# Optimization experiments

Measured on AMD Instinct MI355X. Metric: run time of the kernel, lower is better.

The kernel has to match this reference:

```python
import jax, jax.numpy as jnp
import numpy as np

MIN_NORM = 1e-15
BALL_EPS_F32 = 0.004  # BALL_EPS[torch.float32]


def _norm(x):
    return jnp.maximum(jnp.linalg.norm(x, axis=-1, keepdims=True), MIN_NORM)


def project(x, c=1.0):
    norm = _norm(x)
    maxnorm = (1.0 - BALL_EPS_F32) / (c ** 0.5)
    return jnp.where(norm > maxnorm, x / norm * maxnorm, x)


def expmap0(u, c=1.0):
    sqrt_c = c ** 0.5
    un = _norm(u)
    gamma = jnp.tanh(jnp.clip(sqrt_c * un, -15.0, 15.0)) * u / (sqrt_c * un)
    return project(gamma, c)


def artanh(x):
    x = jnp.clip(x, -1.0 + 1e-5, 1.0 - 1e-5)
    return 0.5 * (jnp.log1p(x) - jnp.log1p(-x))


def logmap0(y, c=1.0):
    sqrt_c = c ** 0.5
    yn = _norm(y)
    return y / yn / sqrt_c * artanh(sqrt_c * yn)


def mobius_add(x, y, c=1.0):
    x2 = jnp.sum(x * x, axis=-1, keepdims=True)
    y2 = jnp.sum(y * y, axis=-1, keepdims=True)
    xy = jnp.sum(x * y, axis=-1, keepdims=True)
    num = (1 + 2 * c * xy + c * y2) * x + (1 - c * x2) * y
    denom = 1 + 2 * c * xy + (c ** 2) * x2 * y2
    return num / jnp.maximum(denom, MIN_NORM)


def p_exp_map(v):
    nv = jnp.maximum(jnp.linalg.norm(v, axis=-1, keepdims=True), 1e-10)
    return jnp.tanh(nv) * v / nv


def setup_inputs() -> dict:
    key = jax.random.key(0)
    ks = jax.random.split(key, 16)
    E, N, B = 1_000_000, 100_000, 512
    n_rel, D, A = 200, 64, 5
    R = 2 * n_rel + 1  # 401

    q_sub = jax.random.randint(ks[0], (B,), 0, N, dtype=jnp.int32)
    q_rel = jax.random.randint(ks[1], (B,), 0, R, dtype=jnp.int32)
    hidden = jax.random.normal(ks[2], (N, D), dtype=jnp.float32)

    r_idx = jax.random.randint(ks[3], (E,), 0, B, dtype=jnp.int32)
    rel = jax.random.randint(ks[4], (E,), 0, R, dtype=jnp.int32)
    sub = jax.random.randint(ks[5], (E,), 0, N, dtype=jnp.int32)
    obj = jax.random.randint(ks[6], (E,), 0, N, dtype=jnp.int32)
    dummy = jnp.zeros((E,), dtype=jnp.int32)
    edges = jnp.stack([r_idx, dummy, rel, dummy, sub, obj], axis=1)  # [E,6]

    s = 1.0 / np.sqrt(D)
    sa = 1.0 / np.sqrt(A)
    rela_embed = jax.random.normal(ks[7], (R, D), dtype=jnp.float32)
    query_embed = jax.random.normal(ks[8], (R, D), dtype=jnp.float32)
    Ws = jax.random.uniform(ks[9], (A, D), jnp.float32, -s, s)
    Wr = jax.random.uniform(ks[10], (A, D), jnp.float32, -s, s)
    Wqr_w = jax.random.uniform(ks[11], (A, D), jnp.float32, -s, s)
    Wqr_b = jax.random.uniform(ks[12], (A,), jnp.float32, -s, s)
    walpha_w = jax.random.uniform(ks[13], (1, A), jnp.float32, -sa, sa)
    walpha_b = jax.random.uniform(ks[14], (1,), jnp.float32, -sa, sa)
    Wh = jax.random.uniform(ks[15], (D, D), jnp.float32, -s, s)

    return {
        "q_sub": q_sub, "q_rel": q_rel, "hidden": hidden, "edges": edges,
        "n_node": N, "old_nodes_new_idx": jax.random.randint(jax.random.fold_in(key, 99), (100,), 0, N, dtype=jnp.int32),
        "rela_embed": rela_embed, "query_embed": query_embed,
        "Ws": Ws, "Wr": Wr, "Wqr_w": Wqr_w, "Wqr_b": Wqr_b,
        "walpha_w": walpha_w, "walpha_b": walpha_b, "Wh": Wh,
    }


def reference(q_sub, q_rel, hidden, edges, n_node, old_nodes_new_idx,
              rela_embed, query_embed, Ws, Wr, Wqr_w, Wqr_b,
              walpha_w, walpha_b, Wh):
    sub = edges[:, 4]
    rel = edges[:, 2]
    obj = edges[:, 5]
    r_idx = edges[:, 0]

    hs = hidden[sub]                     # [E, D] gather
    hr = rela_embed[rel]                 # [E, D]
    h_qr = query_embed[q_rel][r_idx]     # [E, D]

    # attention (note: bilinear/non_linear branch in the original is dead code)
    pre = hs @ Ws.T + hr @ Wr.T + (h_qr @ Wqr_w.T + Wqr_b)   # [E, A]
    alpha = jax.nn.sigmoid(jax.nn.relu(pre) @ walpha_w.T + walpha_b)  # [E, 1]

    hr_h = expmap0(hr, 1.0)
    hs_h = expmap0(hs, 1.0)
    message = logmap0(project(mobius_add(hs_h, hr_h, 1.0), 1.0), 1.0)
    message = alpha * message            # [E, D]

    message_agg = jax.ops.segment_sum(message, obj, num_segments=n_node)  # [N, D]
    a = message_agg @ Wh.T
    a = p_exp_map(a)
    hidden_new = logmap0(a, 1.0)         # act is identity
    return hidden_new
```

## Files before the change

kernel.cpp:

```cpp
#include <hip/hip_runtime.h>
#include <hip/hip_bf16.h>
#include <hip/hip_fp16.h>


__device__ __forceinline__ float wave_sum(float v) {
#pragma unroll
    for (int off = 32; off > 0; off >>= 1) v += __shfl_xor(v, off, 64);
    return v;
}

__device__ __forceinline__ float frcp(float x) {
#if __has_builtin(__builtin_amdgcn_rcpf)
    return __builtin_amdgcn_rcpf(x);
#else
    return 1.f / x;
#endif
}
__device__ __forceinline__ float fsqrt_(float x) {
#if __has_builtin(__builtin_amdgcn_sqrtf)
    return __builtin_amdgcn_sqrtf(x);
#else
    return sqrtf(x);
#endif
}
__device__ __forceinline__ float flog2_(float x) {
#if __has_builtin(__builtin_amdgcn_logf)
    return __builtin_amdgcn_logf(x);
#else
    return log2f(x);
#endif
}
__device__ __forceinline__ float fexp2_(float x) {
#if __has_builtin(__builtin_amdgcn_exp2f)
    return __builtin_amdgcn_exp2f(x);
#else
    return exp2f(x);
#endif
}
__device__ __forceinline__ float ftanh_pos(float x) {
    return 1.f - 2.f * frcp(fexp2_(x * 2.885390082f) + 1.f);
}

__device__ __forceinline__ unsigned pk2(float a, float b) {
    __half2 h = __floats2half2_rn(a, b);
    return __builtin_bit_cast(unsigned, h);
}
__device__ __forceinline__ float2 upk2(unsigned u) {
    __half2 h = __builtin_bit_cast(__half2, u);
    return __half22float2(h);
}

__device__ __forceinline__ void expmap0_scale(float norm, float& s, float& x2) {
    const float maxn = 1.0f - 0.004f;
    float un = fmaxf(norm, 1e-15f);
    float th = ftanh_pos(fminf(un, 15.0f));
    float gs = th * frcp(un);
    float ng = gs * norm;
    float ps = ng > maxn ? maxn * frcp(ng) : 1.0f;
    s = gs * ps;
    float sn = s * norm;
    x2 = sn * sn;
}

__device__ __forceinline__ float2 edge_coef(
    unsigned hu_lo, unsigned hu_hi, unsigned yu_lo, unsigned yu_hi,
    uint4 hsa, uint4 hra, uint4 pqa, const float* wa, float wb) {
    float2 hs01 = upk2(hsa.x), hs23 = upk2(hsa.y), hs4 = upk2(hsa.z), hsxs = upk2(hsa.w);
    float2 hr01 = upk2(hra.x), hr23 = upk2(hra.y), hr4 = upk2(hra.z), hry = upk2(hra.w);
    float2 pq01 = upk2(pqa.x), pq23 = upk2(pqa.y), pq4 = upk2(pqa.z);
    float x2 = hsxs.x, s = hsxs.y, y2 = hry.x;

    float2 hl = upk2(hu_lo), hh = upk2(hu_hi);
    float2 yl = upk2(yu_lo), yh = upk2(yu_hi);

    float p = hl.x * yl.x;
    p = fmaf(hl.y, yl.y, p);
    p = fmaf(hh.x, yh.x, p);
    p = fmaf(hh.y, yh.y, p);
    p += __shfl_xor(p, 1, 64);
    p += __shfl_xor(p, 2, 64);
    p += __shfl_xor(p, 4, 64);
    p += __shfl_xor(p, 8, 64);
    float xy = p * s;

    float z = wb;
    z = fmaf(fmaxf(hs01.x + hr01.x + pq01.x, 0.f), wa[0], z);
    z = fmaf(fmaxf(hs01.y + hr01.y + pq01.y, 0.f), wa[1], z);
    z = fmaf(fmaxf(hs23.x + hr23.x + pq23.x, 0.f), wa[2], z);
    z = fmaf(fmaxf(hs23.y + hr23.y + pq23.y, 0.f), wa[3], z);
    z = fmaf(fmaxf(hs4.x + hr4.x + pq4.x, 0.f), wa[4], z);
    float alpha = frcp(1.f + fexp2_(z * -1.44269504f));

    float Af  = 1.f + 2.f * xy + y2;
    float Bf  = 1.f - x2;
    float den = fmaxf(1.f + 2.f * xy + x2 * y2, 1e-15f);
    float inv = frcp(den);
    float nm2 = fmaxf(fmaf(Af * Af, x2, fmaf(2.f * Af * Bf, xy, Bf * Bf * y2)), 0.f);
    float nm  = fsqrt_(nm2) * inv;
    const float maxn = 1.0f - 0.004f;
    float ps  = nm > maxn ? maxn * frcp(nm) : 1.f;
    float yn  = fmaxf(fminf(nm, maxn), 1e-15f);
    float ratio = (1.f + yn) * frcp(1.f - yn);
    float art = 0.34657359f * flog2_(ratio);
    float k  = inv * ps * alpha * art * frcp(yn);
    return make_float2(k * Af * s, k * Bf);
}

__device__ __forceinline__ void edge_to_global(
    unsigned hu_lo, unsigned hu_hi, unsigned yu_lo, unsigned yu_hi,
    uint4 hsa, uint4 hra, uint4 pqa, const float* wa, float wb,
    bool act, __half2* dst ) {
    float2 c = edge_coef(hu_lo, hu_hi, yu_lo, yu_hi, hsa, hra, pqa, wa, wb);
    float2 hl = upk2(hu_lo), hh = upk2(hu_hi);
    float2 yl = upk2(yu_lo), yh = upk2(yu_hi);
    __half2 q_lo = __floats2half2_rn(fmaf(c.x, hl.x, c.y * yl.x), fmaf(c.x, hl.y, c.y * yl.y));
    __half2 q_hi = __floats2half2_rn(fmaf(c.x, hh.x, c.y * yh.x), fmaf(c.x, hh.y, c.y * yh.y));
    if (act) {
        unsafeAtomicAdd(dst, q_lo);
        unsafeAtomicAdd(dst + 16, q_hi);
    }
}

__global__ void prep_fused16(const int* __restrict__ q_rel,
                             const float* __restrict__ query_embed,
                             const float* __restrict__ Wqr_w,
                             const float* __restrict__ Wqr_b,
                             const float* __restrict__ rela_embed,
                             const float* __restrict__ Wr,
                             const float* __restrict__ hidden,
                             const float* __restrict__ Ws,
                             const int* __restrict__ edges,
                             __half* __restrict__ hidden16,
                             uint4* __restrict__ hs_aux16,
                             __half* __restrict__ hr_h16,
                             uint4* __restrict__ hr_aux16,
                             uint4* __restrict__ preq16,
                             __half* __restrict__ agg16,
                             unsigned long long* __restrict__ packed,
                             int N, int R, int B, int E, int zero_agg) {
    int wid = (blockIdx.x * blockDim.x + threadIdx.x) >> 6;
    int lane = threadIdx.x & 63;
    int nwaves = (N + 3) >> 2;
    if (wid < nwaves) {
        int q = lane >> 4, j = lane & 15;
        int n = wid * 4 + q;
        bool act = n < N;
        int nc = act ? n : N - 1;

        float4 u = *(const float4*)(hidden + (size_t)nc * 64 + 4 * j);
        float4 w0 = *(const float4*)(Ws + 0 * 64 + 4 * j);
        float4 w1 = *(const float4*)(Ws + 1 * 64 + 4 * j);
        float4 w2 = *(const float4*)(Ws + 2 * 64 + 4 * j);
        float4 w3 = *(const float4*)(Ws + 3 * 64 + 4 * j);
        float4 w4 = *(const float4*)(Ws + 4 * 64 + 4 * j);

#define DOT4(a, b) (fmaf((a).x, (b).x, fmaf((a).y, (b).y, fmaf((a).z, (b).z, (a).w * (b).w))))
        float p0 = DOT4(u, u);
        float p1 = DOT4(u, w0);
        float p2 = DOT4(u, w1);
        float p3 = DOT4(u, w2);
        float p4 = DOT4(u, w3);
        float p5 = DOT4(u, w4);
#undef DOT4
#pragma unroll
        for (int off = 1; off < 16; off <<= 1) {
            p0 += __shfl_xor(p0, off, 64);
            p1 += __shfl_xor(p1, off, 64);
            p2 += __shfl_xor(p2, off, 64);
            p3 += __shfl_xor(p3, off, 64);
            p4 += __shfl_xor(p4, off, 64);
            p5 += __shfl_xor(p5, off, 64);
        }
        float s, x2;
        expmap0_scale(fsqrt_(p0), s, x2);
        if (act) {
            uint2 hp; hp.x = pk2(u.x, u.y); hp.y = pk2(u.z, u.w);
            *(uint2*)(hidden16 + (size_t)n * 64 + 4 * j) = hp;
            if (zero_agg) {
                uint2 zz; zz.x = 0u; zz.y = 0u;
                ((uint2*)(agg16 + (size_t)n * 64))[j] = zz;
            }
            if (j == 0) {
                uint4 o; o.x = pk2(p1, p2); o.y = pk2(p3, p4); o.z = pk2(p5, 0.f); o.w = pk2(x2, s);
                hs_aux16[n] = o;
            }
        }
        return;
    }
    int w2 = wid - nwaves;
    if (w2 < R) {
        int r = w2;
        float u = rela_embed[r * 64 + lane];
        float p0 = u * u;
        float p1 = u * Wr[0 * 64 + lane];
        float p2 = u * Wr[1 * 64 + lane];
        float p3 = u * Wr[2 * 64 + lane];
        float p4 = u * Wr[3 * 64 + lane];
        float p5 = u * Wr[4 * 64 + lane];
#pragma unroll
        for (int off = 1; off < 64; off <<= 1) {
            p0 += __shfl_xor(p0, off, 64);
            p1 += __shfl_xor(p1, off, 64);
            p2 += __shfl_xor(p2, off, 64);
            p3 += __shfl_xor(p3, off, 64);
            p4 += __shfl_xor(p4, off, 64);
            p5 += __shfl_xor(p5, off, 64);
        }
        float s, y2;
        expmap0_scale(fsqrt_(p0), s, y2);
        hr_h16[r * 64 + lane] = __float2half(s * u);
        if (lane == 0) {
            uint4 o; o.x = pk2(p1, p2); o.y = pk2(p3, p4); o.z = pk2(p5, 0.f); o.w = pk2(y2, 0.f);
            hr_aux16[r] = o;
        }
        return;
    }
    int w3 = w2 - R;
    if (w3 < B) {
        int b = w3;
        int qr = q_rel[b];
        float q = query_embed[qr * 64 + lane];
        float p1 = q * Wqr_w[0 * 64 + lane];
        float p2 = q * Wqr_w[1 * 64 + lane];
        float p3 = q * Wqr_w[2 * 64 + lane];
        float p4 = q * Wqr_w[3 * 64 + lane];
        float p5 = q * Wqr_w[4 * 64 + lane];
#pragma unroll
        for (int off = 1; off < 64; off <<= 1) {
            p1 += __shfl_xor(p1, off, 64);
            p2 += __shfl_xor(p2, off, 64);
            p3 += __shfl_xor(p3, off, 64);
            p4 += __shfl_xor(p4, off, 64);
            p5 += __shfl_xor(p5, off, 64);
        }
        if (lane == 0) {
            uint4 o;
            o.x = pk2(p1 + Wqr_b[0], p2 + Wqr_b[1]);
            o.y = pk2(p3 + Wqr_b[2], p4 + Wqr_b[3]);
            o.z = pk2(p5 + Wqr_b[4], 0.f);
            o.w = pk2(0.f, 0.f);
            preq16[b] = o;
        }
        return;
    }
    int w4 = w3 - B;
    int e = w4 * 64 + lane;
    if (e < E) {
        const int* er = edges + (size_t)e * 6;
        int ri  = er[0];
        int rel = er[2];
        int sub = er[4];
        int obj = er[5];
        unsigned long long pk = (unsigned long long)(unsigned)(obj & 0x1ffff)
            | ((unsigned long long)(unsigned)(sub & 0x1ffff) << 17)
            | ((unsigned long long)(unsigned)(rel & 0x1ff) << 34)
            | ((unsigned long long)(unsigned)(ri & 0x1ff) << 43);
        __builtin_nontemporal_store(pk, &packed[e]);
    }
}


__global__ void init_cur(int* __restrict__ cur, int NB, int cap) {
    int i = blockIdx.x * blockDim.x + threadIdx.x;
    if (i < NB) cur[i] = i * cap;
    else if (i == NB) cur[i] = 0;
}

__global__ __launch_bounds__(256) void scatter_edges(
    const int* __restrict__ edges, int E, int NB, int cap,
    int* __restrict__ cur,
    unsigned long long* __restrict__ bbuf,
    unsigned long long* __restrict__ ovfbuf, int ovfcap)
{
    __shared__ unsigned long long spk[4096];
    __shared__ int lh[1024];
    __shared__ int lb[1024];
    int t = threadIdx.x;
    int base = blockIdx.x * 4096;
    for (int i = t; i < NB; i += 256) lh[i] = 0;
    __syncthreads();
    int nloc = min(4096, E - base);
    for (int k = t; k < nloc; k += 256) {
        const long long* er = (const long long*)(edges + (size_t)(base + k) * 6);
        long long a = er[0], bq = er[1], cq = er[2];
        int ri = (int)a, rel = (int)bq, sub = (int)cq, obj = (int)(cq >> 32);
        unsigned long long pk = (unsigned long long)(unsigned)(obj & 0x1ffff)
            | ((unsigned long long)(unsigned)(sub & 0x1ffff) << 17)
            | ((unsigned long long)(unsigned)(rel & 0x1ff) << 34)
            | ((unsigned long long)(unsigned)(ri & 0x1ff) << 43);
        spk[k] = pk;
        atomicAdd(&lh[obj >> 7], 1);
    }
    __syncthreads();
    for (int i = t; i < NB; i += 256) {
        int c = lh[i];
        lb[i] = c ? atomicAdd(&cur[i], c) : 0;
    }
    __syncthreads();
    for (int i = t; i < NB; i += 256) lh[i] = 0;
    __syncthreads();
    for (int k = t; k < nloc; k += 256) {
        unsigned long long pk = spk[k];
        int bk = (int)(pk & 0x1ffff) >> 7;
        int rank = atomicAdd(&lh[bk], 1);
        int slot = lb[bk] + rank;
        if (slot < (bk + 1) * cap) {
            bbuf[slot] = pk;
        } else {
            int o = atomicAdd(cur + NB, 1);
            if (o < ovfcap) ovfbuf[o] = pk;
        }
    }
}

__global__ __launch_bounds__(256) void sort_bucket(
    unsigned long long* __restrict__ bbuf,
    const int* __restrict__ cur, int cap,
    int2* __restrict__ nodeoff)
{
    __shared__ unsigned long long spk[4096];
    __shared__ int hist[128];
    __shared__ int pfx[129];
    __shared__ int rk[128];
    int b = blockIdx.x;
    int t = threadIdx.x;
    int start = b * cap;
    int cnt = cur[b] - start;
    if (cnt < 0) cnt = 0;
    if (cnt > cap) cnt = cap;
    if (t < 128) { hist[t] = 0; rk[t] = 0; }
    __syncthreads();
    for (int i = t; i < cnt; i += 256) {
        unsigned long long pk = bbuf[start + i];
        spk[i] = pk;
        atomicAdd(&hist[(int)(pk & 127)], 1);
    }
    __syncthreads();
    if (t == 0) {
        int acc = 0;
#pragma unroll 4
        for (int i = 0; i < 128; ++i) { pfx[i] = acc; acc += hist[i]; }
        pfx[128] = acc;
    }
    __syncthreads();
    if (t < 128) {
        nodeoff[b * 128 + t] = make_int2(start + pfx[t], start + pfx[t + 1]);
    }
    for (int i = t; i < cnt; i += 256) {
        unsigned long long pk = spk[i];
        int loc = (int)(pk & 127);
        int r = atomicAdd(&rk[loc], 1);
        bbuf[start + pfx[loc] + r] = pk;
    }
}

__global__ __launch_bounds__(256) void csr_edge(
    const unsigned long long* __restrict__ bbuf,
    const int2* __restrict__ nodeoff,
    const __half* __restrict__ hidden16,
    const __half* __restrict__ hr_h16,
    const uint4* __restrict__ hs_aux16,
    const uint4* __restrict__ hr_aux16,
    const uint4* __restrict__ preq16,
    const float* __restrict__ walpha_w,
    const float* __restrict__ walpha_b,
    __half* __restrict__ agg16,
    int N, int Ntot)
{
    int t = threadIdx.x;
    int lane = t & 63;
    int g = lane >> 4;
    int j = lane & 15;
    int node = blockIdx.x * 16 + (t >> 6) * 4 + g;
    if (node >= Ntot) return;

    float wa[5];
    wa[0] = walpha_w[0]; wa[1] = walpha_w[1]; wa[2] = walpha_w[2];
    wa[3] = walpha_w[3]; wa[4] = walpha_w[4];
    float wb = walpha_b[0];

    int2 off = nodeoff[node];
    float a0 = 0.f, a1 = 0.f, a2 = 0.f, a3 = 0.f;
    for (int e = off.x; e < off.y; ++e) {
        unsigned long long pk = bbuf[e];
        int sub = (int)((pk >> 17) & 0x1ffff);
        int rel = (int)((pk >> 34) & 0x1ff);
        int ri  = (int)((pk >> 43) & 0x1ff);
        uint4 hsa = hs_aux16[sub], hra = hr_aux16[rel], pqa = preq16[ri];
        const unsigned* hrow = (const unsigned*)(hidden16 + (size_t)sub * 64);
        const unsigned* yrow = (const unsigned*)(hr_h16 + (size_t)rel * 64);
        unsigned hu_lo = hrow[j], hu_hi = hrow[16 + j];
        unsigned yu_lo = yrow[j], yu_hi = yrow[16 + j];
        float2 c = edge_coef(hu_lo, hu_hi, yu_lo, yu_hi, hsa, hra, pqa, wa, wb);
        float2 hl = upk2(hu_lo), hh = upk2(hu_hi);
        float2 yl = upk2(yu_lo), yh = upk2(yu_hi);
        a0 = fmaf(c.x, hl.x, fmaf(c.y, yl.x, a0));
        a1 = fmaf(c.x, hl.y, fmaf(c.y, yl.y, a1));
        a2 = fmaf(c.x, hh.x, fmaf(c.y, yh.x, a2));
        a3 = fmaf(c.x, hh.y, fmaf(c.y, yh.y, a3));
    }
    if (node < N) {
        unsigned* dst = (unsigned*)(agg16 + (size_t)node * 64);
        __builtin_nontemporal_store(pk2(a0, a1), dst + j);
        __builtin_nontemporal_store(pk2(a2, a3), dst + 16 + j);
    }
}

__global__ __launch_bounds__(256) void ovf_edge(
    const unsigned long long* __restrict__ ovfbuf,
    const int* __restrict__ ovfcnt_p, int ovfcap,
    const __half* __restrict__ hidden16,
    const __half* __restrict__ hr_h16,
    const uint4* __restrict__ hs_aux16,
    const uint4* __restrict__ hr_aux16,
    const uint4* __restrict__ preq16,
    const float* __restrict__ walpha_w,
    const float* __restrict__ walpha_b,
    __half2* __restrict__ agg)
{
    int cnt = min(*ovfcnt_p, ovfcap);
    if (cnt <= 0) return;
    int j = threadIdx.x & 15;
    int qid = (blockIdx.x * blockDim.x + threadIdx.x) >> 4;
    int nq = (gridDim.x * blockDim.x) >> 4;
    float wa[5];
    wa[0] = walpha_w[0]; wa[1] = walpha_w[1]; wa[2] = walpha_w[2];
    wa[3] = walpha_w[3]; wa[4] = walpha_w[4];
    float wb = walpha_b[0];
    for (int e = qid; e < cnt; e += nq) {
        unsigned long long pk = ovfbuf[e];
        int obj = (int)(pk & 0x1ffff), sub = (int)((pk >> 17) & 0x1ffff);
        int rel = (int)((pk >> 34) & 0x1ff), ri = (int)((pk >> 43) & 0x1ff);
        uint4 hsa = hs_aux16[sub], hra = hr_aux16[rel], pqa = preq16[ri];
        const unsigned* hrow = (const unsigned*)(hidden16 + (size_t)sub * 64);
        const unsigned* yrow = (const unsigned*)(hr_h16 + (size_t)rel * 64);
        edge_to_global(hrow[j], hrow[16 + j], yrow[j], yrow[16 + j],
                       hsa, hra, pqa, wa, wb, true, agg + (size_t)obj * 32 + j);
    }
}

__global__ __launch_bounds__(256) void edge_kernel8p(
    const unsigned long long* __restrict__ packed,
    const __half* __restrict__ hidden16,
    const __half* __restrict__ hr_h16,
    const uint4* __restrict__ hs_aux16,
    const uint4* __restrict__ hr_aux16,
    const uint4* __restrict__ preq16,
    const float* __restrict__ walpha_w,
    const float* __restrict__ walpha_b,
    __half2* __restrict__ agg,
    int E)
{
    int wid = (blockIdx.x * blockDim.x + threadIdx.x) >> 6;
    int lane = threadIdx.x & 63;
    int g = lane >> 4;
    int j = lane & 15;

    int e0 = wid * 8 + g;
    int e1 = wid * 8 + 4 + g;
    bool act0 = e0 < E, act1 = e1 < E;

    unsigned long long p0 = __builtin_nontemporal_load(&packed[act0 ? e0 : 0]);
    unsigned long long p1 = __builtin_nontemporal_load(&packed[act1 ? e1 : 0]);
    int obj0 = (int)(p0 & 0x1ffff), sub0 = (int)((p0 >> 17) & 0x1ffff);
    int rel0 = (int)((p0 >> 34) & 0x1ff), r0 = (int)((p0 >> 43) & 0x1ff);
    int obj1 = (int)(p1 & 0x1ffff), sub1 = (int)((p1 >> 17) & 0x1ffff);
    int rel1 = (int)((p1 >> 34) & 0x1ff), r1 = (int)((p1 >> 43) & 0x1ff);

    uint4 hsa0 = hs_aux16[sub0], hra0 = hr_aux16[rel0], pqa0 = preq16[r0];
    uint4 hsa1 = hs_aux16[sub1], hra1 = hr_aux16[rel1], pqa1 = preq16[r1];

    const unsigned* hrow0 = (const unsigned*)(hidden16 + (size_t)sub0 * 64);
    const unsigned* yrow0 = (const unsigned*)(hr_h16 + (size_t)rel0 * 64);
    const unsigned* hrow1 = (const unsigned*)(hidden16 + (size_t)sub1 * 64);
    const unsigned* yrow1 = (const unsigned*)(hr_h16 + (size_t)rel1 * 64);

    float wa[5];
    wa[0] = walpha_w[0]; wa[1] = walpha_w[1]; wa[2] = walpha_w[2];
    wa[3] = walpha_w[3]; wa[4] = walpha_w[4];
    float wb = walpha_b[0];

    edge_to_global(hrow0[j], hrow0[16 + j], yrow0[j], yrow0[16 + j],
                   hsa0, hra0, pqa0, wa, wb, act0, agg + (size_t)obj0 * 32 + j);
    edge_to_global(hrow1[j], hrow1[16 + j], yrow1[j], yrow1[16 + j],
                   hsa1, hra1, pqa1, wa, wb, act1, agg + (size_t)obj1 * 32 + j);
}

__global__ __launch_bounds__(256) void final_gemm16(
    float* __restrict__ out,
    const __half* __restrict__ agg16,
    const float* __restrict__ Wh,
    int N)
{
    __shared__ __half tile[64 * 64];
    int t = threadIdx.x;
    int lane = t & 63;
    int w = t >> 6;

    float wh[64];
    const float4* whr = (const float4*)(Wh + (size_t)lane * 64);
#pragma unroll
    for (int i = 0; i < 16; ++i) {
        float4 v = whr[i];
        wh[4 * i] = v.x; wh[4 * i + 1] = v.y; wh[4 * i + 2] = v.z; wh[4 * i + 3] = v.w;
    }

    int base = blockIdx.x << 6;
    int nrow = min(64, N - base);
    {
        const uint2* src = (const uint2*)(agg16 + (size_t)base * 64);
        uint2* dst = (uint2*)tile;
        int nu2 = nrow * 16;
        for (int i = t; i < nu2; i += 256) dst[i] = src[i];
    }
    __syncthreads();

#pragma unroll 1
    for (int r = 0; r < 16; ++r) {
        int n = base + w * 16 + r;
        if (n >= N) break;
        const uint2* arow = (const uint2*)(tile + (w * 16 + r) * 64);
        float acc = 0.f;
#pragma unroll
        for (int kk = 0; kk < 16; ++kk) {
            uint2 u = arow[kk];
            float2 f0 = upk2(u.x), f1 = upk2(u.y);
            acc = fmaf(f0.x, wh[4 * kk], acc);
            acc = fmaf(f0.y, wh[4 * kk + 1], acc);
            acc = fmaf(f1.x, wh[4 * kk + 2], acc);
            acc = fmaf(f1.y, wh[4 * kk + 3], acc);
        }
        float n2 = wave_sum(acc * acc);
        float na = fsqrt_(n2);
        float nv = fmaxf(na, 1e-10f);
        float pn = ftanh_pos(nv);
        float rinv = frcp(nv);
        float pp = pn * acc * rinv;
        float np = pn * (na * rinv);
        float yn = fmaxf(np, 1e-15f);
        float tt = fminf(yn, 1.f - 1e-5f);
        float ratio = (1.f + tt) * frcp(1.f - tt);
        float art = 0.34657359f * flog2_(ratio);
        __builtin_nontemporal_store(pp * art * frcp(yn), &out[(size_t)n * 64 + lane]);
    }
}


__global__ void prep_small_kernel(const int* __restrict__ q_rel,
                                  const float* __restrict__ query_embed,
                                  const float* __restrict__ Wqr_w,
                                  const float* __restrict__ Wqr_b,
                                  const float* __restrict__ rela_embed,
                                  const float* __restrict__ Wr,
                                  float* __restrict__ hr_h,
                                  float* __restrict__ hr_aux,
                                  float* __restrict__ preq,
                                  int R, int B, int A) {
    int w = (blockIdx.x * blockDim.x + threadIdx.x) >> 6;
    int lane = threadIdx.x & 63;
    if (w < R) {
        int r = w;
        float u = rela_embed[r * 64 + lane];
        float n2 = wave_sum(u * u);
        float s, y2;
        expmap0_scale(fsqrt_(n2), s, y2);
        hr_h[r * 64 + lane] = s * u;
        for (int a = 0; a < A; ++a) {
            float p = wave_sum(u * Wr[a * 64 + lane]);
            if (lane == 0) hr_aux[r * 8 + a] = p;
        }
        if (lane == 0) hr_aux[r * 8 + 6] = y2;
    } else if (w < R + B) {
        int b = w - R;
        int qr = q_rel[b];
        float q = query_embed[qr * 64 + lane];
        for (int a = 0; a < A; ++a) {
            float p = wave_sum(q * Wqr_w[a * 64 + lane]);
            if (lane == 0) preq[b * 8 + a] = p + Wqr_b[a];
        }
    }
}

__global__ void prep_node_kernel(const float* __restrict__ hidden,
                                 const float* __restrict__ Ws,
                                 float* __restrict__ hs_aux, int N, int A) {
    int w = (blockIdx.x * blockDim.x + threadIdx.x) >> 6;
    if (w >= N) return;
    int lane = threadIdx.x & 63;
    float u = hidden[(size_t)w * 64 + lane];
    float n2 = wave_sum(u * u);
    float s, x2;
    expmap0_scale(fsqrt_(n2), s, x2);
    for (int a = 0; a < A; ++a) {
        float p = wave_sum(u * Ws[a * 64 + lane]);
        if (lane == 0) hs_aux[w * 8 + a] = p;
    }
    if (lane == 0) { hs_aux[w * 8 + 6] = x2; hs_aux[w * 8 + 7] = s; }
}

__global__ void edge_kernel_f32(const int* __restrict__ edges,
                                const float* __restrict__ hidden,
                                const float* __restrict__ hr_h,
                                const float* __restrict__ hr_aux,
                                const float* __restrict__ hs_aux,
                                const float* __restrict__ preq,
                                const float* __restrict__ walpha_w,
                                const float* __restrict__ walpha_b,
                                float* __restrict__ agg,
                                int E, int A) {
    int w = (blockIdx.x * blockDim.x + threadIdx.x) >> 6;
    if (w >= E) return;
    int lane = threadIdx.x & 63;
    const int* er = edges + (size_t)w * 6;
    int r_idx = er[0], rel = er[2], sub = er[4], obj = er[5];

    float s  = hs_aux[(size_t)sub * 8 + 7];
    float x2 = hs_aux[(size_t)sub * 8 + 6];
    float h  = hidden[(size_t)sub * 64 + lane];
    float x  = h * s;
    float y  = hr_h[(size_t)rel * 64 + lane];
    float y2 = hr_aux[(size_t)rel * 8 + 6];
    float xy = wave_sum(x * y);

    float z = walpha_b[0];
    for (int a = 0; a < A; ++a) {
        float pre = hs_aux[(size_t)sub * 8 + a] + hr_aux[(size_t)rel * 8 + a] + preq[(size_t)r_idx * 8 + a];
        z += fmaxf(pre, 0.f) * walpha_w[a];
    }
    float alpha = frcp(1.f + fexp2_(z * -1.44269504f));

    float Af = 1.f + 2.f * xy + y2;
    float Bf = 1.f - x2;
    float den = fmaxf(1.f + 2.f * xy + x2 * y2, 1e-15f);
    float inv = frcp(den);
    float nm2 = fmaxf(Af * Af * x2 + 2.f * Af * Bf * xy + Bf * Bf * y2, 0.f);
    float nm = fsqrt_(nm2) * inv;
    const float maxn = 1.0f - 0.004f;
    float ps = nm > maxn ? maxn * frcp(nm) : 1.f;
    float yn = fmaxf(fminf(nm, maxn), 1e-15f);
    float ratio = (1.f + yn) * frcp(1.f - yn);
    float art = 0.34657359f * flog2_(ratio);
    float k = inv * ps * alpha * art * frcp(yn);
    float msg = fmaf(k * Af * s, h, k * Bf * y);
    unsafeAtomicAdd(agg + (size_t)obj * 64 + lane, msg);
}

__global__ void final_kernel_f32(float* __restrict__ out,
                                 const float* __restrict__ Wh,
                                 int N) {
    __shared__ float WhT[64 * 64];
    int t = threadIdx.x;
    for (int i = t; i < 64 * 64; i += blockDim.x) {
        int row = i >> 6, col = i & 63;
        WhT[col * 64 + row] = Wh[i];
    }
    __syncthreads();

    int lane = t & 63;
    int wl = t >> 6;
    int wpb = blockDim.x >> 6;
    int wg = blockIdx.x * wpb + wl;
    int wstride = gridDim.x * wpb;

    for (int n = wg; n < N; n += wstride) {
        float v = out[(size_t)n * 64 + lane];
        float a = 0.f;
#pragma unroll
        for (int k = 0; k < 64; ++k)
            a = fmaf(__shfl(v, k, 64), WhT[k * 64 + lane], a);

        float n2 = wave_sum(a * a);
        float na = fsqrt_(n2);
        float nv = fmaxf(na, 1e-10f);
        float pn = tanhf(nv);
        float rinv = frcp(nv);
        float pp = pn * a * rinv;
        float np = pn * (na * rinv);
        float yn = fmaxf(np, 1e-15f);
        float tt = fminf(yn, 1.f - 1e-5f);
        float ratio = (1.f + tt) * frcp(1.f - tt);
        float art = 0.34657359f * flog2_(ratio);
        out[(size_t)n * 64 + lane] = pp * art * frcp(yn);
    }
}

extern "C" void kernel_launch(void* const* d_in, const int* in_sizes, int n_in,
                              void* d_out, int out_size, void* d_ws, size_t ws_size,
                              hipStream_t stream) {
    const int*   q_rel       = (const int*)d_in[1];
    const float* hidden      = (const float*)d_in[2];
    const int*   edges       = (const int*)d_in[3];
    const float* rela_embed  = (const float*)d_in[6];
    const float* query_embed = (const float*)d_in[7];
    const float* Ws          = (const float*)d_in[8];
    const float* Wr          = (const float*)d_in[9];
    const float* Wqr_w       = (const float*)d_in[10];
    const float* Wqr_b       = (const float*)d_in[11];
    const float* walpha_w    = (const float*)d_in[12];
    const float* walpha_b    = (const float*)d_in[13];
    const float* Wh          = (const float*)d_in[14];

    const int D = 64;
    int B = in_sizes[0];
    int E = in_sizes[3] / 6;
    int A = in_sizes[11];
    int R = in_sizes[6] / D;
    int N = out_size / D;

    float* out = (float*)d_out;

    size_t agg_b    = (size_t)N * 128;
    size_t hid16_b  = (size_t)N * 128;
    size_t hsaux_b  = (size_t)N * 16;
    size_t hrh_b    = (size_t)R * 128;
    size_t hraux_b  = (size_t)R * 16;
    size_t preq_b   = (size_t)B * 16;
    size_t need16   = agg_b + hid16_b + hsaux_b + hrh_b + hraux_b + preq_b;
    size_t packed_b = (size_t)E * 8;
    size_t need_pk  = need16 + packed_b;

    int NB = (N + 127) >> 7;
    int Ntot = NB * 128;
    int cap = (NB > 0) ? 2 * ((E + NB - 1) / NB) : 512;
    if (cap < 512) cap = 512;
    int ovfcap = 65536;
    size_t bbuf_b = (size_t)NB * (size_t)cap * 8;
    size_t cur_b  = (((size_t)NB + 1) * 4 + 15) & ~(size_t)15;
    size_t noff_b = (size_t)Ntot * 8;
    size_t ovf_b  = (size_t)ovfcap * 8;
    size_t need_csr = need16 + bbuf_b + cur_b + noff_b + ovf_b;

    bool fields_ok = (N > 0) && (N <= 131072) && (R <= 512) && (B <= 512);
    bool csr_ok = (A == 5) && fields_ok && (NB <= 1024) && (E > 0) &&
                  (cap <= 4096) && ((long long)NB * cap < (1LL << 31)) &&
                  (ws_size >= need_csr);
    bool pkpath = (A == 5) && fields_ok && (ws_size >= need_pk);

    if (csr_ok) {
        char* base = (char*)d_ws;
        __half* agg16    = (__half*)base;            base += agg_b;
        __half* hidden16 = (__half*)base;            base += hid16_b;
        uint4*  hs_aux16 = (uint4*)base;             base += hsaux_b;
        __half* hr_h16   = (__half*)base;            base += hrh_b;
        uint4*  hr_aux16 = (uint4*)base;             base += hraux_b;
        uint4*  preq16   = (uint4*)base;             base += preq_b;
        unsigned long long* bbuf = (unsigned long long*)base; base += bbuf_b;
        int* cur = (int*)base;                       base += cur_b;
        int2* nodeoff = (int2*)base;                 base += noff_b;
        unsigned long long* ovfbuf = (unsigned long long*)base;

        init_cur<<<(NB + 1 + 255) / 256, 256, 0, stream>>>(cur, NB, cap);

        int nwaves = (N + 3) / 4;
        int total_waves = nwaves + R + B;
        prep_fused16<<<(total_waves + 3) / 4, 256, 0, stream>>>(
            q_rel, query_embed, Wqr_w, Wqr_b, rela_embed, Wr,
            hidden, Ws, edges, hidden16, hs_aux16, hr_h16, hr_aux16, preq16,
            agg16, (unsigned long long*)nullptr, N, R, B, 0, 0);

        scatter_edges<<<(E + 4095) / 4096, 256, 0, stream>>>(
            edges, E, NB, cap, cur, bbuf, ovfbuf, ovfcap);

        sort_bucket<<<NB, 256, 0, stream>>>(bbuf, cur, cap, nodeoff);

        csr_edge<<<(Ntot + 15) / 16, 256, 0, stream>>>(
            bbuf, nodeoff, hidden16, hr_h16, hs_aux16, hr_aux16, preq16,
            walpha_w, walpha_b, agg16, N, Ntot);

        ovf_edge<<<64, 256, 0, stream>>>(
            ovfbuf, cur + NB, ovfcap, hidden16, hr_h16, hs_aux16, hr_aux16,
            preq16, walpha_w, walpha_b, (__half2*)agg16);

        int ntiles = (N + 63) / 64;
        final_gemm16<<<ntiles, 256, 0, stream>>>(out, agg16, Wh, N);
    } else if (pkpath) {
        char* base = (char*)d_ws;
        __half2* agg      = (__half2*)base;          base += agg_b;
        __half*  hidden16 = (__half*)base;           base += hid16_b;
        uint4*   hs_aux16 = (uint4*)base;            base += hsaux_b;
        __half*  hr_h16   = (__half*)base;           base += hrh_b;
        uint4*   hr_aux16 = (uint4*)base;            base += hraux_b;
        uint4*   preq16   = (uint4*)base;            base += preq_b;
        unsigned long long* packed = (unsigned long long*)base;

        int nwaves = (N + 3) / 4;
        int ewavesP = (E + 63) / 64;
        int total_waves = nwaves + R + B + ewavesP;
        prep_fused16<<<(total_waves + 3) / 4, 256, 0, stream>>>(
            q_rel, query_embed, Wqr_w, Wqr_b, rela_embed, Wr,
            hidden, Ws, edges, hidden16, hs_aux16, hr_h16, hr_aux16, preq16,
            (__half*)agg, packed, N, R, B, E, 1);

        int ewaves = (E + 7) / 8;
        edge_kernel8p<<<(ewaves + 3) / 4, 256, 0, stream>>>(
            packed, hidden16, hr_h16, hs_aux16, hr_aux16, preq16,
            walpha_w, walpha_b, agg, E);

        int ntiles = (N + 63) / 64;
        final_gemm16<<<ntiles, 256, 0, stream>>>(out, (const __half*)agg, Wh, N);
    } else {
        float* hs_aux = (float*)d_ws;
        float* hr_h   = hs_aux + (size_t)N * 8;
        float* hr_aux = hr_h + (size_t)R * 64;
        float* preq   = hr_aux + (size_t)R * 8;

        (void)hipMemsetAsync(d_out, 0, (size_t)out_size * sizeof(float), stream);

        int waves_small = R + B;
        prep_small_kernel<<<(waves_small * 64 + 255) / 256, 256, 0, stream>>>(
            q_rel, query_embed, Wqr_w, Wqr_b, rela_embed, Wr,
            hr_h, hr_aux, preq, R, B, A);

        prep_node_kernel<<<(N + 3) / 4, 256, 0, stream>>>(hidden, Ws, hs_aux, N, A);

        edge_kernel_f32<<<(E + 3) / 4, 256, 0, stream>>>(
            edges, hidden, hr_h, hr_aux, hs_aux, preq,
            walpha_w, walpha_b, out, E, A);

        final_kernel_f32<<<1024, 256, 0, stream>>>(out, Wh, N);
    }
}
```

Baseline: 163.2 us.

## Process CSR node edges four-wide per wave with fp32 aux tables and fused cur init

The CSR edge kernel now assigns one node per wave and has its four 16-lane groups process four edges at a time, combining partial sums with cross-group shuffles. Per-node load imbalance and the serial per-edge loop latency should shrink. The per-edge auxiliary projections (hs/hr/query) are now also stored as fp32 float4 pairs, so the edge kernel skips half-precision unpacking at the cost of more gather bytes. The separate init_cur launch is folded into the prep kernel to save one launch, and grid size grows four times.

```diff
diff --git a/kernel.cpp b/kernel.cpp
--- a/kernel.cpp
+++ b/kernel.cpp
@@ -109,7 +109,7 @@
 __device__ __forceinline__ void edge_to_global(
     unsigned hu_lo, unsigned hu_hi, unsigned yu_lo, unsigned yu_hi,
     uint4 hsa, uint4 hra, uint4 pqa, const float* wa, float wb,
-    bool act, __half2* dst ) {
+    bool act, __half2* dst) {
     float2 c = edge_coef(hu_lo, hu_hi, yu_lo, yu_hi, hsa, hra, pqa, wa, wb);
     float2 hl = upk2(hu_lo), hh = upk2(hu_hi);
     float2 yl = upk2(yu_lo), yh = upk2(yu_hi);
@@ -119,6 +119,47 @@
         unsafeAtomicAdd(dst, q_lo);
         unsafeAtomicAdd(dst + 16, q_hi);
     }
+}
+
+__device__ __forceinline__ float2 edge_coef32(
+    unsigned hu_lo, unsigned hu_hi, unsigned yu_lo, unsigned yu_hi,
+    float4 hsA, float4 hsB, float4 hrA, float4 hrB, float4 pqA, float pq5,
+    const float* wa, float wb) {
+    float x2 = hsB.z, s = hsB.w, y2 = hrB.z;
+    float2 hl = upk2(hu_lo), hh = upk2(hu_hi);
+    float2 yl = upk2(yu_lo), yh = upk2(yu_hi);
+
+    float p = hl.x * yl.x;
+    p = fmaf(hl.y, yl.y, p);
+    p = fmaf(hh.x, yh.x, p);
+    p = fmaf(hh.y, yh.y, p);
+    p += __shfl_xor(p, 1, 64);
+    p += __shfl_xor(p, 2, 64);
+    p += __shfl_xor(p, 4, 64);
+    p += __shfl_xor(p, 8, 64);
+    float xy = p * s;
+
+    float z = wb;
+    z = fmaf(fmaxf(hsA.x + hrA.x + pqA.x, 0.f), wa[0], z);
+    z = fmaf(fmaxf(hsA.y + hrA.y + pqA.y, 0.f), wa[1], z);
+    z = fmaf(fmaxf(hsA.z + hrA.z + pqA.z, 0.f), wa[2], z);
+    z = fmaf(fmaxf(hsA.w + hrA.w + pqA.w, 0.f), wa[3], z);
+    z = fmaf(fmaxf(hsB.x + hrB.x + pq5, 0.f), wa[4], z);
+    float alpha = frcp(1.f + fexp2_(z * -1.44269504f));
+
+    float Af  = 1.f + 2.f * xy + y2;
+    float Bf  = 1.f - x2;
+    float den = fmaxf(1.f + 2.f * xy + x2 * y2, 1e-15f);
+    float inv = frcp(den);
+    float nm2 = fmaxf(fmaf(Af * Af, x2, fmaf(2.f * Af * Bf, xy, Bf * Bf * y2)), 0.f);
+    float nm  = fsqrt_(nm2) * inv;
+    const float maxn = 1.0f - 0.004f;
+    float ps  = nm > maxn ? maxn * frcp(nm) : 1.f;
+    float yn  = fmaxf(fminf(nm, maxn), 1e-15f);
+    float ratio = (1.f + yn) * frcp(1.f - yn);
+    float art = 0.34657359f * flog2_(ratio);
+    float k  = inv * ps * alpha * art * frcp(yn);
+    return make_float2(k * Af * s, k * Bf);
 }
 
 __global__ void prep_fused16(const int* __restrict__ q_rel,
@@ -135,9 +176,14 @@
                              __half* __restrict__ hr_h16,
                              uint4* __restrict__ hr_aux16,
                              uint4* __restrict__ preq16,
+                             float4* __restrict__ hs_aux32,
+                             float4* __restrict__ hr_aux32,
+                             float4* __restrict__ preq32,
                              __half* __restrict__ agg16,
                              unsigned long long* __restrict__ packed,
-                             int N, int R, int B, int E, int zero_agg) {
+                             int* __restrict__ cur,
+                             int N, int R, int B, int E, int NB, int cap,
+                             int zero_agg) {
     int wid = (blockIdx.x * blockDim.x + threadIdx.x) >> 6;
     int lane = threadIdx.x & 63;
     int nwaves = (N + 3) >> 2;
@@ -183,6 +229,10 @@
             if (j == 0) {
                 uint4 o; o.x = pk2(p1, p2); o.y = pk2(p3, p4); o.z = pk2(p5, 0.f); o.w = pk2(x2, s);
                 hs_aux16[n] = o;
+                if (hs_aux32) {
+                    hs_aux32[(size_t)n * 2]     = make_float4(p1, p2, p3, p4);
+                    hs_aux32[(size_t)n * 2 + 1] = make_float4(p5, 0.f, x2, s);
+                }
             }
         }
         return;
@@ -212,6 +262,10 @@
         if (lane == 0) {
             uint4 o; o.x = pk2(p1, p2); o.y = pk2(p3, p4); o.z = pk2(p5, 0.f); o.w = pk2(y2, 0.f);
             hr_aux16[r] = o;
+            if (hr_aux32) {
+                hr_aux32[(size_t)r * 2]     = make_float4(p1, p2, p3, p4);
+                hr_aux32[(size_t)r * 2 + 1] = make_float4(p5, 0.f, y2, 0.f);
+            }
         }
         return;
     }
@@ -234,16 +288,25 @@
             p5 += __shfl_xor(p5, off, 64);
         }
         if (lane == 0) {
+            float b1 = p1 + Wqr_b[0], b2 = p2 + Wqr_b[1], b3 = p3 + Wqr_b[2];
+            float b4 = p4 + Wqr_b[3], b5 = p5 + Wqr_b[4];
             uint4 o;
-            o.x = pk2(p1 + Wqr_b[0], p2 + Wqr_b[1]);
-            o.y = pk2(p3 + Wqr_b[2], p4 + Wqr_b[3]);
-            o.z = pk2(p5 + Wqr_b[4], 0.f);
-            o.w = pk2(0.f, 0.f);
+            o.x = pk2(b1, b2); o.y = pk2(b3, b4); o.z = pk2(b5, 0.f); o.w = pk2(0.f, 0.f);
             preq16[b] = o;
+            if (preq32) {
+                preq32[(size_t)b * 2]     = make_float4(b1, b2, b3, b4);
+                preq32[(size_t)b * 2 + 1] = make_float4(b5, 0.f, 0.f, 0.f);
+            }
         }
         return;
     }
     int w4 = w3 - B;
+    if (cur) {
+        int i = w4 * 64 + lane;
+        if (i < NB) cur[i] = i * cap;
+        else if (i == NB) cur[i] = 0;
+        return;
+    }
     int e = w4 * 64 + lane;
     if (e < E) {
         const int* er = edges + (size_t)e * 6;
@@ -259,12 +322,6 @@
     }
 }
 
-
-__global__ void init_cur(int* __restrict__ cur, int NB, int cap) {
-    int i = blockIdx.x * blockDim.x + threadIdx.x;
-    if (i < NB) cur[i] = i * cap;
-    else if (i == NB) cur[i] = 0;
-}
 
 __global__ __launch_bounds__(256) void scatter_edges(
     const int* __restrict__ edges, int E, int NB, int cap,
@@ -354,14 +411,14 @@
     }
 }
 
-__global__ __launch_bounds__(256) void csr_edge(
+__global__ __launch_bounds__(256) void csr_edge_w(
     const unsigned long long* __restrict__ bbuf,
     const int2* __restrict__ nodeoff,
     const __half* __restrict__ hidden16,
     const __half* __restrict__ hr_h16,
-    const uint4* __restrict__ hs_aux16,
-    const uint4* __restrict__ hr_aux16,
-    const uint4* __restrict__ preq16,
+    const float4* __restrict__ hs_aux32,
+    const float4* __restrict__ hr_aux32,
+    const float4* __restrict__ preq32,
     const float* __restrict__ walpha_w,
     const float* __restrict__ walpha_b,
     __half* __restrict__ agg16,
@@ -371,7 +428,7 @@
     int lane = t & 63;
     int g = lane >> 4;
     int j = lane & 15;
-    int node = blockIdx.x * 16 + (t >> 6) * 4 + g;
+    int node = blockIdx.x * 4 + (t >> 6);
     if (node >= Ntot) return;
 
     float wa[5];
@@ -381,25 +438,38 @@
 
     int2 off = nodeoff[node];
     float a0 = 0.f, a1 = 0.f, a2 = 0.f, a3 = 0.f;
-    for (int e = off.x; e < off.y; ++e) {
-        unsigned long long pk = bbuf[e];
+    for (int base = off.x; base < off.y; base += 4) {
+        int e = base + g;
+        bool act = e < off.y;
+        int ec = act ? e : off.y - 1;
+        unsigned long long pk = bbuf[ec];
         int sub = (int)((pk >> 17) & 0x1ffff);
         int rel = (int)((pk >> 34) & 0x1ff);
         int ri  = (int)((pk >> 43) & 0x1ff);
-        uint4 hsa = hs_aux16[sub], hra = hr_aux16[rel], pqa = preq16[ri];
+        float4 hsA = hs_aux32[(size_t)sub * 2], hsB = hs_aux32[(size_t)sub * 2 + 1];
+        float4 hrA = hr_aux32[(size_t)rel * 2], hrB = hr_aux32[(size_t)rel * 2 + 1];
+        float4 pqA = preq32[(size_t)ri * 2],   pqB = preq32[(size_t)ri * 2 + 1];
         const unsigned* hrow = (const unsigned*)(hidden16 + (size_t)sub * 64);
         const unsigned* yrow = (const unsigned*)(hr_h16 + (size_t)rel * 64);
         unsigned hu_lo = hrow[j], hu_hi = hrow[16 + j];
         unsigned yu_lo = yrow[j], yu_hi = yrow[16 + j];
-        float2 c = edge_coef(hu_lo, hu_hi, yu_lo, yu_hi, hsa, hra, pqa, wa, wb);
+        float2 c = edge_coef32(hu_lo, hu_hi, yu_lo, yu_hi,
+                               hsA, hsB, hrA, hrB, pqA, pqB.x, wa, wb);
+        float gate = act ? 1.f : 0.f;
+        float cx = c.x * gate, cy = c.y * gate;
         float2 hl = upk2(hu_lo), hh = upk2(hu_hi);
         float2 yl = upk2(yu_lo), yh = upk2(yu_hi);
-        a0 = fmaf(c.x, hl.x, fmaf(c.y, yl.x, a0));
-        a1 = fmaf(c.x, hl.y, fmaf(c.y, yl.y, a1));
-        a2 = fmaf(c.x, hh.x, fmaf(c.y, yh.x, a2));
-        a3 = fmaf(c.x, hh.y, fmaf(c.y, yh.y, a3));
-    }
-    if (node < N) {
+        a0 = fmaf(cx, hl.x, fmaf(cy, yl.x, a0));
+        a1 = fmaf(cx, hl.y, fmaf(cy, yl.y, a1));
+        a2 = fmaf(cx, hh.x, fmaf(cy, yh.x, a2));
+        a3 = fmaf(cx, hh.y, fmaf(cy, yh.y, a3));
+    }
+    a0 += __shfl_xor(a0, 16, 64); a0 += __shfl_xor(a0, 32, 64);
+    a1 += __shfl_xor(a1, 16, 64); a1 += __shfl_xor(a1, 32, 64);
+    a2 += __shfl_xor(a2, 16, 64); a2 += __shfl_xor(a2, 32, 64);
+    a3 += __shfl_xor(a3, 16, 64); a3 += __shfl_xor(a3, 32, 64);
+
+    if (node < N && g == 0) {
         unsigned* dst = (unsigned*)(agg16 + (size_t)node * 64);
         __builtin_nontemporal_store(pk2(a0, a1), dst + j);
         __builtin_nontemporal_store(pk2(a2, a3), dst + 16 + j);
@@ -709,15 +779,18 @@
 
     float* out = (float*)d_out;
 
-    size_t agg_b    = (size_t)N * 128;
-    size_t hid16_b  = (size_t)N * 128;
-    size_t hsaux_b  = (size_t)N * 16;
-    size_t hrh_b    = (size_t)R * 128;
-    size_t hraux_b  = (size_t)R * 16;
-    size_t preq_b   = (size_t)B * 16;
-    size_t need16   = agg_b + hid16_b + hsaux_b + hrh_b + hraux_b + preq_b;
-    size_t packed_b = (size_t)E * 8;
-    size_t need_pk  = need16 + packed_b;
+    size_t agg_b     = (size_t)N * 128;
+    size_t hid16_b   = (size_t)N * 128;
+    size_t hsaux_b   = (size_t)N * 16;
+    size_t hrh_b     = (size_t)R * 128;
+    size_t hraux_b   = (size_t)R * 16;
+    size_t preq_b    = (size_t)B * 16;
+    size_t hsaux32_b = (size_t)N * 32;
+    size_t hraux32_b = (size_t)R * 32;
+    size_t preq32_b  = (size_t)B * 32;
+    size_t need16    = agg_b + hid16_b + hsaux_b + hrh_b + hraux_b + preq_b;
+    size_t packed_b  = (size_t)E * 8;
+    size_t need_pk   = need16 + packed_b;
 
     int NB = (N + 127) >> 7;
     int Ntot = NB * 128;
@@ -728,7 +801,8 @@
     size_t cur_b  = (((size_t)NB + 1) * 4 + 15) & ~(size_t)15;
     size_t noff_b = (size_t)Ntot * 8;
     size_t ovf_b  = (size_t)ovfcap * 8;
-    size_t need_csr = need16 + bbuf_b + cur_b + noff_b + ovf_b;
+    size_t need_csr = need16 + hsaux32_b + hraux32_b + preq32_b +
+                      bbuf_b + cur_b + noff_b + ovf_b;
 
     bool fields_ok = (N > 0) && (N <= 131072) && (R <= 512) && (B <= 512);
     bool csr_ok = (A == 5) && fields_ok && (NB <= 1024) && (E > 0) &&
@@ -744,27 +818,30 @@
         __half* hr_h16   = (__half*)base;            base += hrh_b;
         uint4*  hr_aux16 = (uint4*)base;             base += hraux_b;
         uint4*  preq16   = (uint4*)base;             base += preq_b;
+        float4* hs_aux32 = (float4*)base;            base += hsaux32_b;
+        float4* hr_aux32 = (float4*)base;            base += hraux32_b;
+        float4* preq32   = (float4*)base;            base += preq32_b;
         unsigned long long* bbuf = (unsigned long long*)base; base += bbuf_b;
         int* cur = (int*)base;                       base += cur_b;
         int2* nodeoff = (int2*)base;                 base += noff_b;
         unsigned long long* ovfbuf = (unsigned long long*)base;
 
-        init_cur<<<(NB + 1 + 255) / 256, 256, 0, stream>>>(cur, NB, cap);
-
         int nwaves = (N + 3) / 4;
-        int total_waves = nwaves + R + B;
+        int curwaves = (NB + 1 + 63) / 64;
+        int total_waves = nwaves + R + B + curwaves;
         prep_fused16<<<(total_waves + 3) / 4, 256, 0, stream>>>(
             q_rel, query_embed, Wqr_w, Wqr_b, rela_embed, Wr,
             hidden, Ws, edges, hidden16, hs_aux16, hr_h16, hr_aux16, preq16,
-            agg16, (unsigned long long*)nullptr, N, R, B, 0, 0);
+            hs_aux32, hr_aux32, preq32, agg16,
+            (unsigned long long*)nullptr, cur, N, R, B, 0, NB, cap, 0);
 
         scatter_edges<<<(E + 4095) / 4096, 256, 0, stream>>>(
             edges, E, NB, cap, cur, bbuf, ovfbuf, ovfcap);
 
         sort_bucket<<<NB, 256, 0, stream>>>(bbuf, cur, cap, nodeoff);
 
-        csr_edge<<<(Ntot + 15) / 16, 256, 0, stream>>>(
-            bbuf, nodeoff, hidden16, hr_h16, hs_aux16, hr_aux16, preq16,
+        csr_edge_w<<<(Ntot + 3) / 4, 256, 0, stream>>>(
+            bbuf, nodeoff, hidden16, hr_h16, hs_aux32, hr_aux32, preq32,
             walpha_w, walpha_b, agg16, N, Ntot);
 
         ovf_edge<<<64, 256, 0, stream>>>(
@@ -789,7 +866,8 @@
         prep_fused16<<<(total_waves + 3) / 4, 256, 0, stream>>>(
             q_rel, query_embed, Wqr_w, Wqr_b, rela_embed, Wr,
             hidden, Ws, edges, hidden16, hs_aux16, hr_h16, hr_aux16, preq16,
-            (__half*)agg, packed, N, R, B, E, 1);
+            (float4*)nullptr, (float4*)nullptr, (float4*)nullptr, (__half*)agg,
+            packed, (int*)nullptr, N, R, B, E, 0, 0, 1);
 
         int ewaves = (E + 7) / 8;
         edge_kernel8p<<<(ewaves + 3) / 4, 256, 0, stream>>>(
```

Measured after the change: 157.0 us. 3.8% less time.
